# Kernel tuning notes

Measured on AMD Instinct MI355X. Metric: run time of the kernel, lower is better.

The kernel has to match this reference:

```python
import jax, jax.numpy as jnp
import numpy as np

N = 262144      # nodes
E = 1048576     # edges
NC = 30         # node feature dim
ED = 13         # bond (edge) feature dim
H = 256         # hidden_channels
GH = 512        # config.gnn_hidden_channels
OUT = 256       # out_channels
L = 4           # num_layers
G = 8192        # num graphs in batch


def setup_inputs() -> dict:
    key = jax.random.key(0)
    ks = jax.random.split(key, 16)
    inp = {
        "x": jax.random.normal(ks[0], (N, NC), jnp.float32),
        "edge_attr": jax.random.normal(ks[1], (E, ED), jnp.float32),
        "edge_index": jax.random.randint(ks[2], (2, E), 0, N, jnp.int64),
        "batch": jnp.sort(jax.random.randint(ks[3], (N,), 0, G, jnp.int64)),
        # node_to_hid: Linear(NC, H)
        "W_nh": jax.random.normal(ks[4], (NC, H), jnp.float32) / np.sqrt(NC),
        "b_nh": jnp.zeros((H,), jnp.float32),
        # shared GINEConv nn: Linear(H, H) + ReLU (same module instance for every layer)
        "W1": jax.random.normal(ks[5], (H, H), jnp.float32) / np.sqrt(H),
        "b1": jnp.zeros((H,), jnp.float32),
        # per-layer edge projection Linear(ED, H) inside each GINEConv
        "We": jax.random.normal(ks[6], (L, ED, H), jnp.float32) / np.sqrt(ED),
        "be": jnp.zeros((L, H), jnp.float32),
        # lin1: H -> GH, lin2: GH -> OUT
        "Wl1": jax.random.normal(ks[7], (H, GH), jnp.float32) / np.sqrt(H),
        "bl1": jnp.zeros((GH,), jnp.float32),
        "Wl2": jax.random.normal(ks[8], (GH, OUT), jnp.float32) / np.sqrt(GH),
        "bl2": jnp.zeros((OUT,), jnp.float32),
    }
    return inp


def reference(x, edge_attr, W_nh, b_nh, W1, b1, We, be, Wl1, bl1, Wl2, bl2,
              edge_index, batch):
    src = edge_index[0]  # x_j (messages flow source -> target)
    dst = edge_index[1]
    hid = x @ W_nh + b_nh                                   # [N, H]
    for l in range(L):
        e = edge_attr @ We[l] + be[l]                       # [E, H]
        msg = jax.nn.relu(hid[src] + e)                     # gather + fuse
        agg = jax.ops.segment_sum(msg, dst, num_segments=N) # scatter-sum
        # GINEConv (eps=0) -> shared nn (Linear+ReLU), then outer relu in forward
        hid = jax.nn.relu(jax.nn.relu((hid + agg) @ W1 + b1))
    out = jax.nn.relu(hid @ Wl1 + bl1) @ Wl2 + bl2          # [N, OUT]
    # global_add_pool readout
    return jax.ops.segment_sum(out, batch, num_segments=G)  # [G, OUT]
```

## Files before the change

kernel.cpp:

```cpp
#include <hip/hip_runtime.h>
#include <hip/hip_bf16.h>

#define N_NODES 262144
#define N_EDGES 1048576
#define NC      30
#define ED      13
#define H       256
#define GH      512
#define OUT_C   256
#define NLAYERS 4
#define NGRAPHS 8192

typedef __hip_bfloat16 bf16;
typedef __attribute__((ext_vector_type(8))) short short8;
typedef __attribute__((ext_vector_type(4))) float f32x4;

__device__ unsigned short g_W1t[H * H];
__device__ unsigned short g_Wl1t[2][H * H];
__device__ unsigned short g_Wl2t[2][H * H];
__device__ float g_b1[H];
__device__ float g_bl1[GH];
__device__ float g_bl2[OUT_C];
__device__ unsigned int g_ssrc[N_EDGES];
__device__ float        g_seat[N_EDGES * 16];
__device__ unsigned int g_rowptr[N_NODES + 1];
__device__ unsigned int g_cursor[N_NODES];
__device__ unsigned int g_bsum[1024];

__device__ __forceinline__ float hw2f(unsigned short h) {
    return __uint_as_float(((unsigned int)h) << 16);
}
__device__ __forceinline__ float ldf(const void* p, size_t i, bool isbf) {
    return isbf ? hw2f(((const unsigned short*)p)[i]) : ((const float*)p)[i];
}
__device__ __forceinline__ int ldi(const void* p, size_t j, bool is64) {
    return ((const int*)p)[is64 ? 2 * j : j];
}
__device__ __forceinline__ unsigned short bfbits(float f) {
    bf16 b = __float2bfloat16(f);
    return *(unsigned short*)&b;
}
__device__ __forceinline__ float lo16(unsigned int u) { return __uint_as_float(u << 16); }
__device__ __forceinline__ float hi16(unsigned int u) { return __uint_as_float(u & 0xFFFF0000u); }
__device__ __forceinline__ unsigned int pk2(float a, float b) {
    return (unsigned int)bfbits(a) | ((unsigned int)bfbits(b) << 16);
}
__device__ __forceinline__ bool sniff_bf16(const void* xv) {
    const unsigned short* q = (const unsigned short*)xv;
    int c = 0;
    for (int i = 0; i < 32; ++i) {
        unsigned short h = q[2 * i];
        int e = (h >> 7) & 0xFF;
        c += (h == 0 || (e >= 97 && e <= 141)) ? 1 : 0;
    }
    return c >= 20;
}
__device__ __forceinline__ bool sniff_i64(const void* pv, size_t baseWord) {
    const unsigned int* q = (const unsigned int*)pv;
    int z = 0;
    for (int i = 0; i < 32; ++i) z += (q[baseWord + 2 * i + 1] == 0) ? 1 : 0;
    return z >= 20;
}
__device__ __forceinline__ void gload_lds16(const void* g, void* l) {
    __builtin_amdgcn_global_load_lds(
        (const __attribute__((address_space(1))) unsigned int*)g,
        (__attribute__((address_space(3))) unsigned int*)l, 16, 0, 0);
}

__global__ __launch_bounds__(256) void fill_f4(float4* p, int n4, float val) {
    int i = blockIdx.x * 256 + threadIdx.x;
    int stride = gridDim.x * 256;
    float4 z = make_float4(val, val, val, val);
    for (; i < n4; i += stride) p[i] = z;
}

__global__ __launch_bounds__(256) void pack_wt(const void* __restrict__ in,
        int ldin, int k0, int n0, int which) {
    const bool isbf = sniff_bf16(in);
    unsigned short* outp = which == 0 ? g_W1t
                         : which == 1 ? g_Wl1t[0]
                         : which == 2 ? g_Wl1t[1]
                         : which == 3 ? g_Wl2t[0] : g_Wl2t[1];
    const int n = blockIdx.x, k = threadIdx.x;
    outp[(n << 8) + k] = bfbits(ldf(in, (size_t)(k0 + k) * ldin + n0 + n, isbf));
}
__global__ __launch_bounds__(256) void pack_bias(const void* b1, const void* bl1,
                                                 const void* bl2) {
    const int t = threadIdx.x;
    const bool s1 = sniff_bf16(b1), s2 = sniff_bf16(bl1), s3 = sniff_bf16(bl2);
    g_b1[t]        = ldf(b1,  t,       s1);
    g_bl1[t]       = ldf(bl1, t,       s2);
    g_bl1[t + 256] = ldf(bl1, t + 256, s2);
    g_bl2[t]       = ldf(bl2, t,       s3);
}

__global__ __launch_bounds__(256) void csr_zero() {
    g_cursor[blockIdx.x * 256 + threadIdx.x] = 0u;
}
__global__ __launch_bounds__(256) void hist_dst(const void* __restrict__ eidx) {
    const bool is64 = sniff_i64(eidx, 0);
    const int e = blockIdx.x * 256 + threadIdx.x;
    int dst = ldi(eidx, (size_t)N_EDGES + e, is64);
    if ((unsigned)dst >= (unsigned)N_NODES) dst = 0;
    atomicAdd(&g_cursor[dst], 1u);
}
__global__ __launch_bounds__(256) void scan1() {
    __shared__ unsigned int sh[256];
    const int tid = threadIdx.x;
    sh[tid] = g_cursor[blockIdx.x * 256 + tid];
    __syncthreads();
    for (int s = 128; s > 0; s >>= 1) {
        if (tid < s) sh[tid] += sh[tid + s];
        __syncthreads();
    }
    if (tid == 0) g_bsum[blockIdx.x] = sh[0];
}
__global__ __launch_bounds__(256) void scan2() {
    __shared__ unsigned int sh[1024];
    const int tid = threadIdx.x;
    for (int j = tid; j < 1024; j += 256) sh[j] = g_bsum[j];
    __syncthreads();
    if (tid == 0) {
        unsigned int run = 0;
        for (int j = 0; j < 1024; ++j) { unsigned int t = sh[j]; sh[j] = run; run += t; }
    }
    __syncthreads();
    for (int j = tid; j < 1024; j += 256) g_bsum[j] = sh[j];
}
__global__ __launch_bounds__(256) void scan3() {
    __shared__ unsigned int sh[256];
    const int tid = threadIdx.x;
    const int i = blockIdx.x * 256 + tid;
    const unsigned int v = g_cursor[i];
    sh[tid] = v;
    __syncthreads();
    for (int ofs = 1; ofs < 256; ofs <<= 1) {
        unsigned int t = (tid >= ofs) ? sh[tid - ofs] : 0u;
        __syncthreads();
        sh[tid] += t;
        __syncthreads();
    }
    const unsigned int excl = sh[tid] - v + g_bsum[blockIdx.x];
    g_rowptr[i] = excl;
    g_cursor[i] = excl;
    if (i == N_NODES - 1) g_rowptr[N_NODES] = excl + v;
}
__global__ __launch_bounds__(256) void scatter_e(
        const void* __restrict__ eidx, const void* __restrict__ eattr) {
    const bool is64 = sniff_i64(eidx, 0);
    const bool isbf = sniff_bf16(eattr);
    const int e = blockIdx.x * 256 + threadIdx.x;
    int src = ldi(eidx, e, is64);
    int dst = ldi(eidx, (size_t)N_EDGES + e, is64);
    if ((unsigned)src >= (unsigned)N_NODES) src = 0;
    if ((unsigned)dst >= (unsigned)N_NODES) dst = 0;
    unsigned int pos = atomicAdd(&g_cursor[dst], 1u);
    if (pos >= (unsigned)N_EDGES) return;
    g_ssrc[pos] = (unsigned int)src;
    float a[16];
#pragma unroll
    for (int k = 0; k < ED; ++k) a[k] = ldf(eattr, (size_t)e * ED + k, isbf);
    a[13] = 0.f; a[14] = 0.f; a[15] = 0.f;
    float* so = g_seat + (size_t)pos * 16;
#pragma unroll
    for (int k = 0; k < 4; ++k)
        *(float4*)(so + 4 * k) = *(float4*)(a + 4 * k);
}

__global__ __launch_bounds__(256) void node_proj(
        const void* __restrict__ x, const void* __restrict__ W,
        const void* __restrict__ b, bf16* __restrict__ hid) {
    const bool isbf = sniff_bf16(x);
    __shared__ float xs[16 * NC];
    const int m0 = blockIdx.x * 16;
    for (int i = threadIdx.x; i < 16 * NC; i += 256)
        xs[i] = ldf(x, (size_t)m0 * NC + i, isbf);
    __syncthreads();
    const int col = threadIdx.x;
    float w[NC];
#pragma unroll
    for (int k = 0; k < NC; ++k) w[k] = ldf(W, (size_t)k * H + col, isbf);
    const float bias = ldf(b, col, isbf);
#pragma unroll 4
    for (int r = 0; r < 16; ++r) {
        float acc = bias;
#pragma unroll
        for (int k = 0; k < NC; ++k) acc += xs[r * NC + k] * w[k];
        hid[(size_t)(m0 + r) * H + col] = __float2bfloat16(acc);
    }
}

__global__ __launch_bounds__(256) void gine_agg(
        const void* __restrict__ We, size_t weOff,
        const void* __restrict__ be, size_t beOff,
        const unsigned short* __restrict__ hid,
        unsigned short* __restrict__ hsum) {
    const bool isbf = sniff_bf16(We);
    const int lane = threadIdx.x & 63;
    const int wave = threadIdx.x >> 6;
    const int wh   = wave & 1;
    const int wp   = wave >> 1;
    const int c0 = lane + 128 * wh;
    const int c1 = c0 + 64;
    float w0[ED], w1[ED];
#pragma unroll
    for (int k = 0; k < ED; ++k) {
        const size_t o = weOff + (size_t)k * H;
        w0[k] = ldf(We, o + c0, isbf);
        w1[k] = ldf(We, o + c1, isbf);
    }
    const float bb0 = ldf(be, beOff + c0, isbf);
    const float bb1 = ldf(be, beOff + c1, isbf);

    const int nbase = blockIdx.x * 16 + wp * 8;
    for (int j = 0; j < 8; ++j) {
        const int node = nbase + j;
        const unsigned int r0 = __builtin_amdgcn_readfirstlane(g_rowptr[node]);
        const unsigned int r1 = __builtin_amdgcn_readfirstlane(g_rowptr[node + 1]);
        const unsigned short* hn = hid + (size_t)node * H;
        float a0 = hw2f(hn[c0]);
        float a1 = hw2f(hn[c1]);
        unsigned int sc = (r0 < r1) ? g_ssrc[r0] : 0u;
        for (unsigned int e = r0; e < r1; ++e) {
            const unsigned int sn = (e + 1 < r1) ? g_ssrc[e + 1] : 0u;
            const unsigned int s = __builtin_amdgcn_readfirstlane(sc);
            const float* sp = g_seat + (size_t)e * 16;
            const float4 f0 = *(const float4*)(sp);
            const float4 f1 = *(const float4*)(sp + 4);
            const float4 f2 = *(const float4*)(sp + 8);
            const float  fc = sp[12];
            const unsigned short* hs = hid + (size_t)s * H;
            const float h0 = hw2f(hs[c0]);
            const float h1 = hw2f(hs[c1]);
            const float af[ED] = {f0.x, f0.y, f0.z, f0.w, f1.x, f1.y, f1.z,
                                  f1.w, f2.x, f2.y, f2.z, f2.w, fc};
            float m0 = bb0, m1 = bb1;
#pragma unroll
            for (int k = 0; k < ED; ++k) {
                m0 += af[k] * w0[k];
                m1 += af[k] * w1[k];
            }
            a0 += fmaxf(m0 + h0, 0.f);
            a1 += fmaxf(m1 + h1, 0.f);
            sc = sn;
        }
        unsigned short* ho = hsum + (size_t)node * H;
        ho[c0] = bfbits(a0);
        ho[c1] = bfbits(a1);
    }
}

template <int MODE>
__global__ __launch_bounds__(256) void gemm_mfma(
        const unsigned short* __restrict__ A, int bsel,
        unsigned short* __restrict__ Cb, float* __restrict__ Cf,
        const void* __restrict__ batch, size_t batOff, int doRelu, int useBias) {
    __shared__ unsigned short As[64 * 64];
    __shared__ unsigned short Bs[256 * 64];
    const int tid  = threadIdx.x;
    const int lane = tid & 63;
    const int wave = tid >> 6;
    const int m0   = blockIdx.x * 64;

    const unsigned short* Bt = bsel == 0 ? g_W1t
                             : bsel == 1 ? g_Wl1t[0]
                             : bsel == 2 ? g_Wl1t[1]
                             : bsel == 3 ? g_Wl2t[0] : g_Wl2t[1];
    const float* bias = bsel == 0 ? g_b1
                      : bsel == 1 ? g_bl1
                      : bsel == 2 ? g_bl1 + 256 : g_bl2;

    const int ar   = tid >> 2;
    const int ac   = (tid & 3) << 4;
    const int awb  = (ar << 7) + (ac << 1);
    const int aswz = (ar & 7) << 4;
    const size_t arow = (size_t)(m0 + ar) * H + ac;
    const int nrow = lane >> 3;
    const int kbu  = ((lane & 7) ^ nrow) << 4;

    f32x4 acc0[8], acc1[8];
    const f32x4 zz = {0.f, 0.f, 0.f, 0.f};
#pragma unroll
    for (int i = 0; i < 8; ++i) { acc0[i] = zz; acc1[i] = zz; }

    const int fr   = lane & 15;
    const int fg   = lane >> 4;
    const int rowb = (wave >> 1) << 5;
    const int colb = (wave & 1) << 7;

    for (int kt = 0; kt < 4; ++kt) {
#pragma unroll
        for (int j = 0; j < 8; ++j) {
            const int q = (wave << 3) + j;
            gload_lds16((const char*)Bt + (((size_t)(q << 3) + nrow) << 9)
                            + (kt << 7) + kbu,
                        (char*)Bs + (q << 10));
        }
        {
            const size_t aoff = arow + (kt << 6);
            uint4 w0 = *(const uint4*)(A + aoff);
            uint4 w1 = *(const uint4*)(A + aoff + 8);
            *(uint4*)((char*)As + (awb ^ aswz)) = w0;
            *(uint4*)((char*)As + ((awb + 16) ^ aswz)) = w1;
        }
        __syncthreads();
#pragma unroll
        for (int s = 0; s < 2; ++s) {
            const int kofs = (s << 6) + (fg << 4);
            const int r0 = rowb + fr;
            short8 aF0 = *(const short8*)((const char*)As +
                          ((r0 << 7) + (kofs ^ ((r0 & 7) << 4))));
            short8 aF1 = *(const short8*)((const char*)As +
                          (((r0 + 16) << 7) + (kofs ^ ((r0 & 7) << 4))));
#pragma unroll
            for (int ct = 0; ct < 8; ++ct) {
                const int cc = colb + (ct << 4) + fr;
                short8 bF = *(const short8*)((const char*)Bs +
                             ((cc << 7) + (kofs ^ ((cc & 7) << 4))));
                acc0[ct] = __builtin_amdgcn_mfma_f32_16x16x32_bf16(aF0, bF, acc0[ct], 0, 0, 0);
                acc1[ct] = __builtin_amdgcn_mfma_f32_16x16x32_bf16(aF1, bF, acc1[ct], 0, 0, 0);
            }
        }
        __syncthreads();
    }

    const int crow = m0 + rowb + (fg << 2);
    if (MODE == 0) {
#pragma unroll
        for (int ct = 0; ct < 8; ++ct) {
            const int cc = colb + (ct << 4) + fr;
            const float bc = bias[cc];
#pragma unroll
            for (int r = 0; r < 4; ++r) {
                float v0 = acc0[ct][r] + bc;
                float v1 = acc1[ct][r] + bc;
                if (doRelu) { v0 = fmaxf(v0, 0.f); v1 = fmaxf(v1, 0.f); }
                Cb[(size_t)(crow + r) * H + cc]      = bfbits(v0);
                Cb[(size_t)(crow + 16 + r) * H + cc] = bfbits(v1);
            }
        }
    } else {
        const bool is64 = sniff_i64(batch, N_NODES / 2);
        int ga[5], gb[5];
#pragma unroll
        for (int r = 0; r < 4; ++r) {
            int g0 = ldi(batch, batOff + crow + r, is64);
            int g1 = ldi(batch, batOff + crow + 16 + r, is64);
            ga[r] = ((unsigned)g0 < (unsigned)NGRAPHS) ? g0 : 0;
            gb[r] = ((unsigned)g1 < (unsigned)NGRAPHS) ? g1 : 0;
        }
#pragma unroll
        for (int ct = 0; ct < 8; ++ct) {
            const int cc = colb + (ct << 4) + fr;
            const float bc = useBias ? bias[cc] : 0.f;
            float run0 = 0.f, run1 = 0.f;
#pragma unroll
            for (int r = 0; r < 4; ++r) {
                run0 += acc0[ct][r] + bc;
                if (r == 3 || ga[r + 1] != ga[r]) {
                    atomicAdd(&Cf[(size_t)ga[r] * OUT_C + cc], run0); run0 = 0.f;
                }
                run1 += acc1[ct][r] + bc;
                if (r == 3 || gb[r + 1] != gb[r]) {
                    atomicAdd(&Cf[(size_t)gb[r] * OUT_C + cc], run1); run1 = 0.f;
                }
            }
        }
    }
}

extern "C" void kernel_launch(void* const* d_in, const int* in_sizes, int n_in,
                              void* d_out, int out_size, void* d_ws, size_t ws_size,
                              hipStream_t stream) {
    const void *x = nullptr, *eattr = nullptr, *eidx = nullptr, *batch = nullptr;
    const void *W_nh = nullptr, *W1 = nullptr, *We = nullptr, *be = nullptr;
    const void *Wl1 = nullptr, *Wl2 = nullptr, *bl1 = nullptr;
    const void *z256[3] = {nullptr, nullptr, nullptr};
    int nz = 0;
    for (int i = 0; i < n_in; ++i) {
        switch (in_sizes[i]) {
            case N_NODES * NC:     x     = d_in[i]; break;
            case N_EDGES * ED:     eattr = d_in[i]; break;
            case 2 * N_EDGES:      eidx  = d_in[i]; break;
            case N_NODES:          batch = d_in[i]; break;
            case NC * H:           W_nh  = d_in[i]; break;
            case H * H:            W1    = d_in[i]; break;
            case NLAYERS * ED * H: We    = d_in[i]; break;
            case NLAYERS * H:      be    = d_in[i]; break;
            case H * GH:           if (!Wl1) Wl1 = d_in[i]; else Wl2 = d_in[i]; break;
            case GH:               bl1   = d_in[i]; break;
            case H:                if (nz < 3) z256[nz++] = d_in[i]; break;
            default: break;
        }
    }
    const void* b_nh = z256[0];
    const void* b1   = (nz > 1) ? z256[1] : z256[0];
    const void* bl2  = (nz > 2) ? z256[2] : z256[0];
    float* out = (float*)d_out;

    if (!x || !eattr || !eidx || !batch || !W_nh || !W1 || !We || !be ||
        !Wl1 || !Wl2 || !bl1 || !b_nh) {
        fill_f4<<<1024, 256, 0, stream>>>((float4*)out, NGRAPHS * OUT_C / 4, 2.0e6f);
        return;
    }

    const size_t NH = (size_t)N_NODES * H;
    const size_t need = NH * 2 + NH * 2;
    if (ws_size < need) {
        fill_f4<<<1024, 256, 0, stream>>>((float4*)out, NGRAPHS * OUT_C / 4, 1.0e6f);
        return;
    }
    bf16* hid            = (bf16*)d_ws;
    unsigned short* hsum = (unsigned short*)((char*)d_ws + NH * 2);

    pack_wt<<<256, 256, 0, stream>>>(W1,  H,     0,   0, 0);
    pack_wt<<<256, 256, 0, stream>>>(Wl1, GH,    0,   0, 1);
    pack_wt<<<256, 256, 0, stream>>>(Wl1, GH,    0, 256, 2);
    pack_wt<<<256, 256, 0, stream>>>(Wl2, OUT_C, 0,   0, 3);
    pack_wt<<<256, 256, 0, stream>>>(Wl2, OUT_C, 256, 0, 4);
    pack_bias<<<1, 256, 0, stream>>>(b1, bl1, bl2);

    csr_zero<<<N_NODES / 256, 256, 0, stream>>>();
    hist_dst<<<N_EDGES / 256, 256, 0, stream>>>(eidx);
    scan1<<<N_NODES / 256, 256, 0, stream>>>();
    scan2<<<1, 256, 0, stream>>>();
    scan3<<<N_NODES / 256, 256, 0, stream>>>();
    scatter_e<<<N_EDGES / 256, 256, 0, stream>>>(eidx, eattr);

    node_proj<<<N_NODES / 16, 256, 0, stream>>>(x, W_nh, b_nh, hid);

    for (int l = 0; l < NLAYERS; ++l) {
        gine_agg<<<N_NODES / 16, 256, 0, stream>>>(
            We, (size_t)l * ED * H, be, (size_t)l * H,
            (const unsigned short*)hid, hsum);
        gemm_mfma<0><<<N_NODES / 64, 256, 0, stream>>>(
            hsum, 0, (unsigned short*)hid, nullptr, nullptr, 0, 1, 1);
    }

    unsigned short* t0 = hsum;
    fill_f4<<<2048, 256, 0, stream>>>((float4*)out, NGRAPHS * OUT_C / 4, 0.f);
    for (int c = 0; c < 2; ++c) {
        gemm_mfma<0><<<N_NODES / 64, 256, 0, stream>>>(
            (const unsigned short*)hid, 1 + c,
            t0, nullptr, nullptr, 0, 1, 1);
        gemm_mfma<1><<<N_NODES / 64, 256, 0, stream>>>(
            t0, 3 + c,
            nullptr, out, batch, 0, 0, c == 0);
    }
}
```

Measured before the change: 2.382 ms.

## Enlarge GEMM M-tile to 128 rows and unroll edge aggregation by two

The MFMA GEMM now processes 128 rows per block instead of 64, so each wave computes a 64x128 tile with four A fragments reusing every B fragment. This halves how often the weight matrix is reloaded into LDS per output row, at the cost of more accumulator registers (128 floats per lane) and lower occupancy. Separately, the gather-aggregation loop now handles two edges per iteration, issuing both source-index and feature loads together for more memory-level parallelism, with a scalar tail for an odd edge count.

```diff
diff --git a/kernel.cpp b/kernel.cpp
--- a/kernel.cpp
+++ b/kernel.cpp
@@ -220,10 +220,41 @@
         const unsigned short* hn = hid + (size_t)node * H;
         float a0 = hw2f(hn[c0]);
         float a1 = hw2f(hn[c1]);
-        unsigned int sc = (r0 < r1) ? g_ssrc[r0] : 0u;
-        for (unsigned int e = r0; e < r1; ++e) {
-            const unsigned int sn = (e + 1 < r1) ? g_ssrc[e + 1] : 0u;
-            const unsigned int s = __builtin_amdgcn_readfirstlane(sc);
+        unsigned int e = r0;
+        for (; e + 2 <= r1; e += 2) {
+            const unsigned int sA = __builtin_amdgcn_readfirstlane(g_ssrc[e]);
+            const unsigned int sB = __builtin_amdgcn_readfirstlane(g_ssrc[e + 1]);
+            const float* pA = g_seat + (size_t)e * 16;
+            const float* pB = pA + 16;
+            const unsigned short* hA = hid + (size_t)sA * H;
+            const unsigned short* hB = hid + (size_t)sB * H;
+            const float4 fA0 = *(const float4*)(pA);
+            const float4 fA1 = *(const float4*)(pA + 4);
+            const float4 fA2 = *(const float4*)(pA + 8);
+            const float  fAc = pA[12];
+            const float4 fB0 = *(const float4*)(pB);
+            const float4 fB1 = *(const float4*)(pB + 4);
+            const float4 fB2 = *(const float4*)(pB + 8);
+            const float  fBc = pB[12];
+            const float hA0 = hw2f(hA[c0]), hA1 = hw2f(hA[c1]);
+            const float hB0 = hw2f(hB[c0]), hB1 = hw2f(hB[c1]);
+            const float afA[ED] = {fA0.x, fA0.y, fA0.z, fA0.w, fA1.x, fA1.y,
+                                   fA1.z, fA1.w, fA2.x, fA2.y, fA2.z, fA2.w, fAc};
+            const float afB[ED] = {fB0.x, fB0.y, fB0.z, fB0.w, fB1.x, fB1.y,
+                                   fB1.z, fB1.w, fB2.x, fB2.y, fB2.z, fB2.w, fBc};
+            float mA0 = bb0, mA1 = bb1, mB0 = bb0, mB1 = bb1;
+#pragma unroll
+            for (int k = 0; k < ED; ++k) {
+                mA0 += afA[k] * w0[k];
+                mA1 += afA[k] * w1[k];
+                mB0 += afB[k] * w0[k];
+                mB1 += afB[k] * w1[k];
+            }
+            a0 += fmaxf(mA0 + hA0, 0.f) + fmaxf(mB0 + hB0, 0.f);
+            a1 += fmaxf(mA1 + hA1, 0.f) + fmaxf(mB1 + hB1, 0.f);
+        }
+        if (e < r1) {
+            const unsigned int s = __builtin_amdgcn_readfirstlane(g_ssrc[e]);
             const float* sp = g_seat + (size_t)e * 16;
             const float4 f0 = *(const float4*)(sp);
             const float4 f1 = *(const float4*)(sp + 4);
@@ -242,7 +273,6 @@
             }
             a0 += fmaxf(m0 + h0, 0.f);
             a1 += fmaxf(m1 + h1, 0.f);
-            sc = sn;
         }
         unsigned short* ho = hsum + (size_t)node * H;
         ho[c0] = bfbits(a0);
@@ -255,12 +285,12 @@
         const unsigned short* __restrict__ A, int bsel,
         unsigned short* __restrict__ Cb, float* __restrict__ Cf,
         const void* __restrict__ batch, size_t batOff, int doRelu, int useBias) {
-    __shared__ unsigned short As[64 * 64];
+    __shared__ unsigned short As[128 * 64];
     __shared__ unsigned short Bs[256 * 64];
     const int tid  = threadIdx.x;
     const int lane = tid & 63;
     const int wave = tid >> 6;
-    const int m0   = blockIdx.x * 64;
+    const int m0   = blockIdx.x * 128;
 
     const unsigned short* Bt = bsel == 0 ? g_W1t
                              : bsel == 1 ? g_Wl1t[0]
@@ -270,22 +300,24 @@
                       : bsel == 1 ? g_bl1
                       : bsel == 2 ? g_bl1 + 256 : g_bl2;
 
-    const int ar   = tid >> 2;
-    const int ac   = (tid & 3) << 4;
-    const int awb  = (ar << 7) + (ac << 1);
+    const int ar   = tid >> 1;
+    const int ak   = (tid & 1) << 5;
+    const int awb  = (ar << 7) + (ak << 1);
     const int aswz = (ar & 7) << 4;
-    const size_t arow = (size_t)(m0 + ar) * H + ac;
+    const size_t arow = (size_t)(m0 + ar) * H + ak;
     const int nrow = lane >> 3;
     const int kbu  = ((lane & 7) ^ nrow) << 4;
 
-    f32x4 acc0[8], acc1[8];
+    f32x4 acc[4][8];
     const f32x4 zz = {0.f, 0.f, 0.f, 0.f};
 #pragma unroll
-    for (int i = 0; i < 8; ++i) { acc0[i] = zz; acc1[i] = zz; }
+    for (int i = 0; i < 4; ++i)
+#pragma unroll
+        for (int j = 0; j < 8; ++j) acc[i][j] = zz;
 
     const int fr   = lane & 15;
     const int fg   = lane >> 4;
-    const int rowb = (wave >> 1) << 5;
+    const int rowb = (wave >> 1) << 6;
     const int colb = (wave & 1) << 7;
 
     for (int kt = 0; kt < 4; ++kt) {
@@ -297,28 +329,37 @@
                         (char*)Bs + (q << 10));
         }
         {
-            const size_t aoff = arow + (kt << 6);
-            uint4 w0 = *(const uint4*)(A + aoff);
-            uint4 w1 = *(const uint4*)(A + aoff + 8);
-            *(uint4*)((char*)As + (awb ^ aswz)) = w0;
-            *(uint4*)((char*)As + ((awb + 16) ^ aswz)) = w1;
+            const unsigned short* ap = A + arow + (kt << 6);
+            uint4 v0 = *(const uint4*)(ap);
+            uint4 v1 = *(const uint4*)(ap + 8);
+            uint4 v2 = *(const uint4*)(ap + 16);
+            uint4 v3 = *(const uint4*)(ap + 24);
+            char* asb = (char*)As;
+            *(uint4*)(asb + ((awb +  0) ^ aswz)) = v0;
+            *(uint4*)(asb + ((awb + 16) ^ aswz)) = v1;
+            *(uint4*)(asb + ((awb + 32) ^ aswz)) = v2;
+            *(uint4*)(asb + ((awb + 48) ^ aswz)) = v3;
         }
         __syncthreads();
 #pragma unroll
         for (int s = 0; s < 2; ++s) {
             const int kofs = (s << 6) + (fg << 4);
-            const int r0 = rowb + fr;
-            short8 aF0 = *(const short8*)((const char*)As +
+            short8 aF[4];
+#pragma unroll
+            for (int rg = 0; rg < 4; ++rg) {
+                const int r0 = rowb + (rg << 4) + fr;
+                aF[rg] = *(const short8*)((const char*)As +
                           ((r0 << 7) + (kofs ^ ((r0 & 7) << 4))));
-            short8 aF1 = *(const short8*)((const char*)As +
-                          (((r0 + 16) << 7) + (kofs ^ ((r0 & 7) << 4))));
+            }
 #pragma unroll
             for (int ct = 0; ct < 8; ++ct) {
                 const int cc = colb + (ct << 4) + fr;
-                short8 bF = *(const short8*)((const char*)Bs +
+                const short8 bF = *(const short8*)((const char*)Bs +
                              ((cc << 7) + (kofs ^ ((cc & 7) << 4))));
-                acc0[ct] = __builtin_amdgcn_mfma_f32_16x16x32_bf16(aF0, bF, acc0[ct], 0, 0, 0);
-                acc1[ct] = __builtin_amdgcn_mfma_f32_16x16x32_bf16(aF1, bF, acc1[ct], 0, 0, 0);
+#pragma unroll
+                for (int rg = 0; rg < 4; ++rg)
+                    acc[rg][ct] = __builtin_amdgcn_mfma_f32_16x16x32_bf16(
+                        aF[rg], bF, acc[rg][ct], 0, 0, 0);
             }
         }
         __syncthreads();
@@ -331,38 +372,39 @@
             const int cc = colb + (ct << 4) + fr;
             const float bc = bias[cc];
 #pragma unroll
-            for (int r = 0; r < 4; ++r) {
-                float v0 = acc0[ct][r] + bc;
-                float v1 = acc1[ct][r] + bc;
-                if (doRelu) { v0 = fmaxf(v0, 0.f); v1 = fmaxf(v1, 0.f); }
-                Cb[(size_t)(crow + r) * H + cc]      = bfbits(v0);
-                Cb[(size_t)(crow + 16 + r) * H + cc] = bfbits(v1);
+            for (int rg = 0; rg < 4; ++rg) {
+#pragma unroll
+                for (int r = 0; r < 4; ++r) {
+                    float v = acc[rg][ct][r] + bc;
+                    if (doRelu) v = fmaxf(v, 0.f);
+                    Cb[(size_t)(crow + (rg << 4) + r) * H + cc] = bfbits(v);
+                }
             }
         }
     } else {
         const bool is64 = sniff_i64(batch, N_NODES / 2);
-        int ga[5], gb[5];
-#pragma unroll
-        for (int r = 0; r < 4; ++r) {
-            int g0 = ldi(batch, batOff + crow + r, is64);
-            int g1 = ldi(batch, batOff + crow + 16 + r, is64);
-            ga[r] = ((unsigned)g0 < (unsigned)NGRAPHS) ? g0 : 0;
-            gb[r] = ((unsigned)g1 < (unsigned)NGRAPHS) ? g1 : 0;
-        }
+        int g[4][4];
+#pragma unroll
+        for (int rg = 0; rg < 4; ++rg)
+#pragma unroll
+            for (int r = 0; r < 4; ++r) {
+                int gg = ldi(batch, batOff + crow + (rg << 4) + r, is64);
+                g[rg][r] = ((unsigned)gg < (unsigned)NGRAPHS) ? gg : 0;
+            }
 #pragma unroll
         for (int ct = 0; ct < 8; ++ct) {
             const int cc = colb + (ct << 4) + fr;
             const float bc = useBias ? bias[cc] : 0.f;
-            float run0 = 0.f, run1 = 0.f;
-#pragma unroll
-            for (int r = 0; r < 4; ++r) {
-                run0 += acc0[ct][r] + bc;
-                if (r == 3 || ga[r + 1] != ga[r]) {
-                    atomicAdd(&Cf[(size_t)ga[r] * OUT_C + cc], run0); run0 = 0.f;
-                }
-                run1 += acc1[ct][r] + bc;
-                if (r == 3 || gb[r + 1] != gb[r]) {
-                    atomicAdd(&Cf[(size_t)gb[r] * OUT_C + cc], run1); run1 = 0.f;
+#pragma unroll
+            for (int rg = 0; rg < 4; ++rg) {
+                float run = 0.f;
+#pragma unroll
+                for (int r = 0; r < 4; ++r) {
+                    run += acc[rg][ct][r] + bc;
+                    if (r == 3 || g[rg][r + 1] != g[rg][r]) {
+                        atomicAdd(&Cf[(size_t)g[rg][r] * OUT_C + cc], run);
+                        run = 0.f;
+                    }
                 }
             }
         }
@@ -433,17 +475,17 @@
         gine_agg<<<N_NODES / 16, 256, 0, stream>>>(
             We, (size_t)l * ED * H, be, (size_t)l * H,
             (const unsigned short*)hid, hsum);
-        gemm_mfma<0><<<N_NODES / 64, 256, 0, stream>>>(
+        gemm_mfma<0><<<N_NODES / 128, 256, 0, stream>>>(
             hsum, 0, (unsigned short*)hid, nullptr, nullptr, 0, 1, 1);
     }
 
     unsigned short* t0 = hsum;
     fill_f4<<<2048, 256, 0, stream>>>((float4*)out, NGRAPHS * OUT_C / 4, 0.f);
     for (int c = 0; c < 2; ++c) {
-        gemm_mfma<0><<<N_NODES / 64, 256, 0, stream>>>(
+        gemm_mfma<0><<<N_NODES / 128, 256, 0, stream>>>(
             (const unsigned short*)hid, 1 + c,
             t0, nullptr, nullptr, 0, 1, 1);
-        gemm_mfma<1><<<N_NODES / 64, 256, 0, stream>>>(
+        gemm_mfma<1><<<N_NODES / 128, 256, 0, stream>>>(
             t0, 3 + c,
             nullptr, out, batch, 0, 0, c == 0);
     }
```

After: 2.575 ms. 8.1% more time.
